# Performance work log

Hardware: AMD Instinct MI355X
Metric: run time of the kernel (lower is better)

## Reference

```python
import jax, jax.numpy as jnp
import numpy as np

LENGTHS = [1024, 768, 896, 512, 1024, 640, 1024, 768, 512, 896, 1024, 704]  # sum = 9792
EMBED, HEADS = 1024, 16
HDIM = EMBED // HEADS  # 64
ROPE_BASE = 10000.0


def _rotate_half(x):
    half = x.shape[-1] // 2
    return jnp.concatenate([-x[..., half:], x[..., :half]], axis=-1)


def setup_inputs() -> dict:
    key = jax.random.key(0)
    ks = jax.random.split(key, 8)
    T = sum(LENGTHS)
    hidden = jax.random.normal(ks[0], (T, EMBED), jnp.float32)
    # RoPE cos/sin: positions restart at 0 within each packed segment
    pos = np.concatenate([np.arange(l) for l in LENGTHS]).astype(np.float32)  # [T]
    inv_freq = 1.0 / (ROPE_BASE ** (np.arange(0, HDIM, 2, dtype=np.float32) / HDIM))
    freqs = np.outer(pos, inv_freq)                       # [T, HDIM//2]
    emb = np.concatenate([freqs, freqs], axis=-1)         # [T, HDIM]
    cos = jnp.asarray(np.cos(emb), jnp.float32)
    sin = jnp.asarray(np.sin(emb), jnp.float32)
    s = 0.02
    q_w = jax.random.normal(ks[1], (EMBED, EMBED), jnp.float32) * s
    k_w = jax.random.normal(ks[2], (EMBED, EMBED), jnp.float32) * s
    v_w = jax.random.normal(ks[3], (EMBED, EMBED), jnp.float32) * s
    out_w = jax.random.normal(ks[4], (EMBED, EMBED), jnp.float32) * s
    q_b = jax.random.normal(ks[5], (EMBED,), jnp.float32) * s
    v_b = jax.random.normal(ks[6], (EMBED,), jnp.float32) * s
    out_b = jax.random.normal(ks[7], (EMBED,), jnp.float32) * s
    return {
        "hidden_states": hidden, "cos": cos, "sin": sin,
        "q_w": q_w, "q_b": q_b, "k_w": k_w, "v_w": v_w, "v_b": v_b,
        "out_w": out_w, "out_b": out_b,
        "seq_len": jnp.array(LENGTHS, jnp.int32),
        "max_seqlen": 1024,
    }


def reference(hidden_states, cos, sin, q_w, q_b, k_w, v_w, v_b, out_w, out_b,
              seq_len, max_seqlen):
    T, D = hidden_states.shape
    H, Dh = HEADS, D // HEADS
    B = seq_len.shape[0]
    L = max_seqlen  # static python int

    # Projections (torch Linear: y = x @ W.T + b; k_proj has no bias)
    q = (hidden_states @ q_w.T + q_b).reshape(T, H, Dh)
    k = (hidden_states @ k_w.T).reshape(T, H, Dh)
    v = (hidden_states @ v_w.T + v_b).reshape(T, H, Dh)

    # Inline RoPE (cos/sin broadcast over heads)
    c = cos[:, None, :]
    s = sin[:, None, :]
    q = q * c + _rotate_half(q) * s
    k = k * c + _rotate_half(k) * s

    # Gather packed tokens into padded [B, L, H, Dh] (honors ragged structure:
    # no [T, T] dense score matrix, only per-segment [L, L] blocks)
    cu = jnp.concatenate([jnp.zeros((1,), seq_len.dtype), jnp.cumsum(seq_len)])[:-1]  # [B] starts
    ar = jnp.arange(L)
    idx = cu[:, None] + ar[None, :]                 # [B, L] token ids
    valid = ar[None, :] < seq_len[:, None]          # [B, L]
    idxc = jnp.minimum(idx, T - 1)
    qp = q[idxc]                                    # [B, L, H, Dh]
    kp = k[idxc]
    vp = v[idxc]

    scale = 1.0 / jnp.sqrt(jnp.float32(Dh))
    scores = jnp.einsum('blhd,bmhd->bhlm', qp, kp) * scale  # [B, H, L, L]
    causal = ar[:, None] >= ar[None, :]             # [L, L]
    mask = valid[:, None, None, :] & causal[None, None, :, :]
    scores = jnp.where(mask, scores, jnp.float32(-1e30))
    probs = jax.nn.softmax(scores, axis=-1)
    attn = jnp.einsum('bhlm,bmhd->blhd', probs, vp).reshape(B, L, D)

    # Scatter valid tokens back to packed layout [T, D]
    attn = attn * valid[..., None].astype(attn.dtype)
    flat = jnp.zeros((T, D), attn.dtype).at[idxc.reshape(-1)].add(attn.reshape(-1, D))
    return flat @ out_w.T + out_b
```

## Files before the change

### kernel.cpp

```cpp
#include <hip/hip_runtime.h>

typedef __bf16 bf16;
typedef __bf16 bf16x8 __attribute__((ext_vector_type(8)));
typedef __bf16 bf16x4 __attribute__((ext_vector_type(4)));
typedef float  f32x4  __attribute__((ext_vector_type(4)));

#define T_TOTAL 9792
#define EMBED   1024
#define NHEAD   16
#define HDIM    64

__constant__ int c_seq_start[12] = {0,1024,1792,2688,3200,4224,4864,5888,6656,7168,8064,9088};
__constant__ int c_tiles_cum[13] = {0,16,28,42,50,66,76,92,104,112,126,142,153};

typedef __attribute__((address_space(1))) unsigned int gu32;
typedef __attribute__((address_space(3))) unsigned int lu32;

__device__ __forceinline__ void load_lds16(const void* g, void* l) {
    __builtin_amdgcn_global_load_lds((gu32*)g, (lu32*)l, 16, 0, 0);
}

__device__ __forceinline__ f32x4 mfma16(bf16x8 a, bf16x8 b, f32x4 c) {
    return __builtin_amdgcn_mfma_f32_16x16x32_bf16(a, b, c, 0, 0, 0);
}

struct CvtArgs {
    const void* src[10];
    bf16*       dst[10];
    int         n[10];
    int         cum[10];
};

__global__ void to_bf16_fused(CvtArgs a, const unsigned short* __restrict__ disc)
{
    const bool f32 = (disc[0] == 0);
    const int blk = blockIdx.x;
    int seg = 0;
    #pragma unroll
    for (int i = 1; i < 10; ++i) if (blk >= a.cum[i]) seg = i;
    int i0 = (blk - a.cum[seg]) * 2048 + threadIdx.x * 8;
    if (i0 >= a.n[seg]) return;
    bf16x8 o;
    if (f32) {
        const float4* s = (const float4*)((const float*)a.src[seg] + i0);
        float4 x = s[0], y = s[1];
        o[0]=(bf16)x.x; o[1]=(bf16)x.y; o[2]=(bf16)x.z; o[3]=(bf16)x.w;
        o[4]=(bf16)y.x; o[5]=(bf16)y.y; o[6]=(bf16)y.z; o[7]=(bf16)y.w;
    } else {
        o = *(const bf16x8*)((const bf16*)a.src[seg] + i0);
    }
    *(bf16x8*)(a.dst[seg] + i0) = o;
}

__device__ __forceinline__
void gemm_core(const bf16* __restrict__ A, const bf16* __restrict__ W,
               int M, int m0, int n0, f32x4 (&acc)[4][4],
               bf16* lA, bf16* lB)
{
    const int tid  = threadIdx.x;
    const int wave = tid >> 6, lane = tid & 63;
    const int lrow = lane >> 3;
    const int gsw  = (lane & 7) ^ lrow;
    const int ln   = lane & 15, lq = lane >> 4;
    const int e7   = ln & 7;
    const int wm = (wave & 1) * 64,  wn = (wave >> 1) * 64;

    for (int k0 = 0; k0 < 1024; k0 += 64) {
        __syncthreads();
        for (int j = 0; j < 4; ++j) {
            int r = j * 32 + wave * 8;
            int gr = m0 + r + lrow; if (gr > M - 1) gr = M - 1;
            load_lds16(A + (size_t)gr * EMBED + k0 + gsw * 8, &lA[r * 64]);
            load_lds16(W + (size_t)(n0 + r + lrow) * EMBED + k0 + gsw * 8, &lB[r * 64]);
        }
        __syncthreads();
        #pragma unroll
        for (int kb = 0; kb < 2; ++kb) {
            bf16x8 af[4], bfr[4];
            #pragma unroll
            for (int i = 0; i < 4; ++i)
                af[i]  = *(const bf16x8*)&lA[(wm + i * 16 + ln) * 64 + (((kb * 4 + lq) ^ e7) * 8)];
            #pragma unroll
            for (int i = 0; i < 4; ++i)
                bfr[i] = *(const bf16x8*)&lB[(wn + i * 16 + ln) * 64 + (((kb * 4 + lq) ^ e7) * 8)];
            #pragma unroll
            for (int mi = 0; mi < 4; ++mi)
                #pragma unroll
                for (int ni = 0; ni < 4; ++ni)
                    acc[mi][ni] = mfma16(af[mi], bfr[ni], acc[mi][ni]);
        }
    }
}

__device__ __forceinline__ void map_block(int L, int NY, int& x, int& y)
{
    const int per = 8 * NY;
    const int full = 9 * per;
    if (L < full) { int sc = L / per, rem = L % per; x = sc * 8 + (rem & 7); y = rem >> 3; }
    else          { int rem = L - full; x = 72 + rem % 5; y = rem / 5; }
}

__global__ __launch_bounds__(256, 2)
void gemm_qkv(const bf16* __restrict__ A,
              const bf16* __restrict__ Wq, const bf16* __restrict__ Wk,
              const bf16* __restrict__ Wv, const bf16* __restrict__ qb,
              const bf16* __restrict__ vb,
              const bf16* __restrict__ cosb, const bf16* __restrict__ sinb,
              bf16* __restrict__ Cq, bf16* __restrict__ Ck,
              bf16* __restrict__ Vt, int M)
{
    __shared__ __align__(16) bf16 lA[128 * 64];
    __shared__ __align__(16) bf16 lB[128 * 64];

    int x, yy;
    map_block(blockIdx.x, 24, x, yy);
    const int which = yy >> 3;
    const int m0 = x * 128, n0 = (yy & 7) * 128;

    const bf16* W = (which == 0) ? Wq : (which == 1) ? Wk : Wv;
    f32x4 acc[4][4] = {};
    gemm_core(A, W, M, m0, n0, acc, lA, lB);

    const int tid  = threadIdx.x;
    const int wave = tid >> 6, lane = tid & 63;
    const int ln   = lane & 15, lq = lane >> 4;
    const int wm = (wave & 1) * 64,  wn = (wave >> 1) * 64;

    if (which < 2) {
        bf16* C = (which == 0) ? Cq : Ck;
        const bf16* bias = (which == 0) ? qb : nullptr;
        #pragma unroll
        for (int mi = 0; mi < 4; ++mi) {
            int trow = m0 + wm + mi * 16 + lq * 4;
            if (trow >= M) continue;
            #pragma unroll
            for (int ni = 0; ni < 2; ++ni) {
                int d    = ni * 16 + ln;
                int col0 = n0 + wn + d;
                int col1 = col0 + 32;
                float b0 = bias ? (float)bias[col0] : 0.0f;
                float b1 = bias ? (float)bias[col1] : 0.0f;
                #pragma unroll
                for (int r = 0; r < 4; ++r) {
                    int t = trow + r;
                    float c = (float)cosb[t * HDIM + d];
                    float s = (float)sinb[t * HDIM + d];
                    float x0 = acc[mi][ni][r] + b0;
                    float x1 = acc[mi][ni + 2][r] + b1;
                    C[(size_t)t * EMBED + col0] = (bf16)(x0 * c - x1 * s);
                    C[(size_t)t * EMBED + col1] = (bf16)(x1 * c + x0 * s);
                }
            }
        }
    } else {
        const int hd0 = n0 + wn;
        #pragma unroll
        for (int mi = 0; mi < 4; ++mi) {
            int trow = m0 + wm + mi * 16 + lq * 4;
            if (trow >= M) continue;
            #pragma unroll
            for (int ni = 0; ni < 4; ++ni) {
                int d = ni * 16 + ln;
                float bv = (float)vb[hd0 + d];
                bf16x4 o;
                #pragma unroll
                for (int r = 0; r < 4; ++r) o[r] = (bf16)(acc[mi][ni][r] + bv);
                *(bf16x4*)&Vt[(size_t)(hd0 + d) * T_TOTAL + trow] = o;
            }
        }
    }
}

__global__ __launch_bounds__(256, 2)
void gemm_out(const bf16* __restrict__ A, const bf16* __restrict__ W,
              const bf16* __restrict__ bias, void* __restrict__ out, int M,
              const unsigned short* __restrict__ disc)
{
    __shared__ __align__(16) bf16 lA[128 * 64];
    __shared__ __align__(16) bf16 lB[128 * 64];

    int x, yy;
    map_block(blockIdx.x, 8, x, yy);
    const int m0 = x * 128, n0 = yy * 128;

    f32x4 acc[4][4] = {};
    gemm_core(A, W, M, m0, n0, acc, lA, lB);

    const bool f32 = (disc[0] == 0);
    const int tid  = threadIdx.x;
    const int wave = tid >> 6, lane = tid & 63;
    const int ln   = lane & 15, lq = lane >> 4;
    const int wm = (wave & 1) * 64,  wn = (wave >> 1) * 64;

    #pragma unroll
    for (int mi = 0; mi < 4; ++mi) {
        int trow = m0 + wm + mi * 16 + lq * 4;
        if (trow >= M) continue;
        #pragma unroll
        for (int ni = 0; ni < 4; ++ni) {
            int col = n0 + wn + ni * 16 + ln;
            float bv = (float)bias[col];
            #pragma unroll
            for (int r = 0; r < 4; ++r) {
                float v = acc[mi][ni][r] + bv;
                size_t idx = (size_t)(trow + r) * EMBED + col;
                if (f32) ((float*)out)[idx] = v;
                else     ((bf16*)out)[idx]  = (bf16)v;
            }
        }
    }
}

__global__ __launch_bounds__(256, 3)
void attn_kernel(const bf16* __restrict__ Q, const bf16* __restrict__ K,
                 const bf16* __restrict__ Vt, bf16* __restrict__ O)
{
    __shared__ __align__(16) bf16 sK[2][64 * 64];
    __shared__ __align__(16) bf16 sV[2][64 * 64];
    __shared__ __align__(16) bf16 sQP[4 * 16 * 72];

    const int tid  = threadIdx.x;
    const int wave = tid >> 6, lane = tid & 63;
    const int lrow = lane >> 3;
    const int gsw  = (lane & 7) ^ lrow;
    const int ln   = lane & 15, lq = lane >> 4;
    const int e7   = ln & 7;
    const int h = blockIdx.y;

    int b = 0;
    #pragma unroll
    for (int i = 1; i < 13; ++i) if ((int)blockIdx.x >= c_tiles_cum[i]) b = i;
    const int qt = blockIdx.x - c_tiles_cum[b];
    const int t0 = c_seq_start[b] + qt * 64;
    const int kvb0 = c_seq_start[b];

    for (int p = 0; p < 2; ++p) {
        int r = p * 32 + wave * 8;
        load_lds16(Q  + (size_t)(t0 + r + lrow) * EMBED + h * HDIM + gsw * 8, &sQP[r * 64]);
        load_lds16(K  + (size_t)(kvb0 + r + lrow) * EMBED + h * HDIM + gsw * 8, &sK[0][r * 64]);
        load_lds16(Vt + (size_t)(h * HDIM + r + lrow) * T_TOTAL + kvb0 + gsw * 8, &sV[0][r * 64]);
    }

    bf16x8 qf[2];
    f32x4 oacc[4] = {};
    float m_i = -1e30f, l_i = 0.0f;
    const float sc = 0.125f * 1.44269504088896f;
    const int q_loc = wave * 16 + ln;
    bf16* sP = &sQP[wave * 16 * 72];

    for (int j = 0; j <= qt; ++j) {
        __syncthreads();
        const int cur = j & 1;
        if (j == 0) {
            qf[0] = *(const bf16x8*)&sQP[q_loc * 64 + ((0 + lq) ^ e7) * 8];
            qf[1] = *(const bf16x8*)&sQP[q_loc * 64 + ((4 + lq) ^ e7) * 8];
            __syncthreads();
        }
        if (j < qt) {
            const int kvb = kvb0 + (j + 1) * 64;
            const int nxt = cur ^ 1;
            for (int p = 0; p < 2; ++p) {
                int r = p * 32 + wave * 8;
                load_lds16(K  + (size_t)(kvb + r + lrow) * EMBED + h * HDIM + gsw * 8, &sK[nxt][r * 64]);
                load_lds16(Vt + (size_t)(h * HDIM + r + lrow) * T_TOTAL + kvb + gsw * 8, &sV[nxt][r * 64]);
            }
        }

        f32x4 s[4] = {};
        #pragma unroll
        for (int kk = 0; kk < 2; ++kk)
            #pragma unroll
            for (int ni = 0; ni < 4; ++ni) {
                bf16x8 kf = *(const bf16x8*)&sK[cur][(ni * 16 + ln) * 64 + (((kk * 4 + lq) ^ e7) * 8)];
                s[ni] = mfma16(kf, qf[kk], s[ni]);
            }

        float pb[4][4];
        if (j == qt) {
            #pragma unroll
            for (int ni = 0; ni < 4; ++ni)
                #pragma unroll
                for (int r = 0; r < 4; ++r) {
                    int kv = ni * 16 + lq * 4 + r;
                    pb[ni][r] = (kv <= q_loc) ? s[ni][r] * sc : -1e30f;
                }
        } else {
            #pragma unroll
            for (int ni = 0; ni < 4; ++ni)
                #pragma unroll
                for (int r = 0; r < 4; ++r)
                    pb[ni][r] = s[ni][r] * sc;
        }

        float mx = pb[0][0];
        #pragma unroll
        for (int ni = 0; ni < 4; ++ni)
            #pragma unroll
            for (int r = 0; r < 4; ++r) mx = fmaxf(mx, pb[ni][r]);
        mx = fmaxf(mx, __shfl_xor(mx, 16));
        mx = fmaxf(mx, __shfl_xor(mx, 32));
        float mnew  = fmaxf(m_i, mx);
        float alpha = exp2f(m_i - mnew);
        m_i = mnew;

        float rs = 0.0f;
        #pragma unroll
        for (int ni = 0; ni < 4; ++ni)
            #pragma unroll
            for (int r = 0; r < 4; ++r) {
                float pe = exp2f(pb[ni][r] - mnew);
                pb[ni][r] = pe;
                rs += pe;
            }
        rs += __shfl_xor(rs, 16);
        rs += __shfl_xor(rs, 32);
        l_i = l_i * alpha + rs;
        #pragma unroll
        for (int d = 0; d < 4; ++d)
            #pragma unroll
            for (int r = 0; r < 4; ++r) oacc[d][r] *= alpha;

        #pragma unroll
        for (int ni = 0; ni < 4; ++ni) {
            bf16x4 w4;
            #pragma unroll
            for (int r = 0; r < 4; ++r) w4[r] = (bf16)pb[ni][r];
            *(bf16x4*)&sP[ln * 72 + ni * 16 + lq * 4] = w4;
        }
        asm volatile("s_waitcnt lgkmcnt(0)" ::: "memory");

        #pragma unroll
        for (int kk = 0; kk < 2; ++kk) {
            bf16x8 pf = *(const bf16x8*)&sP[ln * 72 + kk * 32 + lq * 8];
            #pragma unroll
            for (int d = 0; d < 4; ++d) {
                bf16x8 vf = *(const bf16x8*)&sV[cur][(d * 16 + ln) * 64 + (((kk * 4 + lq) ^ e7) * 8)];
                oacc[d] = mfma16(vf, pf, oacc[d]);
            }
        }
    }

    const float inv = 1.0f / l_i;
    const size_t row = (size_t)(t0 + q_loc) * EMBED + h * HDIM;
    #pragma unroll
    for (int d = 0; d < 4; ++d) {
        bf16x4 o4;
        #pragma unroll
        for (int r = 0; r < 4; ++r) o4[r] = (bf16)(oacc[d][r] * inv);
        *(bf16x4*)&O[row + d * 16 + lq * 4] = o4;
    }
}

extern "C" void kernel_launch(void* const* d_in, const int* in_sizes, int n_in,
                              void* d_out, int out_size, void* d_ws, size_t ws_size,
                              hipStream_t stream)
{
    const unsigned short* disc = (const unsigned short*)d_in[1];

    const size_t SZ  = (size_t)T_TOTAL * EMBED;
    const size_t CS  = (size_t)T_TOTAL * HDIM;
    const size_t WSZ = (size_t)EMBED * EMBED;

    bf16* p = (bf16*)d_ws;
    bf16* ch   = p; p += SZ;
    bf16* ccos = p; p += CS;
    bf16* csin = p; p += CS;
    bf16* cqw  = p; p += WSZ;
    bf16* ckw  = p; p += WSZ;
    bf16* cvw  = p; p += WSZ;
    bf16* cow  = p; p += WSZ;
    bf16* cqb  = p; p += EMBED;
    bf16* cvb  = p; p += EMBED;
    bf16* cob  = p; p += EMBED;
    bf16* wq   = p; p += SZ;
    bf16* wk   = p; p += SZ;
    bf16* wvt  = p; p += SZ;

    CvtArgs ca;
    const void* srcs[10] = {d_in[0], d_in[1], d_in[2], d_in[3], d_in[5],
                            d_in[6], d_in[8], d_in[4], d_in[7], d_in[9]};
    bf16* dsts[10] = {ch, ccos, csin, cqw, ckw, cvw, cow, cqb, cvb, cob};
    int   ns[10]   = {(int)SZ, (int)CS, (int)CS, (int)WSZ, (int)WSZ,
                      (int)WSZ, (int)WSZ, EMBED, EMBED, EMBED};
    int cum = 0;
    for (int i = 0; i < 10; ++i) {
        ca.src[i] = srcs[i]; ca.dst[i] = dsts[i]; ca.n[i] = ns[i];
        ca.cum[i] = cum;
        cum += (ns[i] + 2047) / 2048;
    }
    to_bf16_fused<<<cum, 256, 0, stream>>>(ca, disc);

    gemm_qkv<<<77 * 24, 256, 0, stream>>>(ch, cqw, ckw, cvw, cqb, cvb,
                                          ccos, csin, wq, wk, wvt, T_TOTAL);
    attn_kernel<<<dim3(153, 16), 256, 0, stream>>>(wq, wk, wvt, wq);
    gemm_out<<<77 * 8, 256, 0, stream>>>(wq, cow, cob, d_out, T_TOTAL, disc);
}
```

Baseline: 283.5 us.

## Process 128 query rows per attention block, remap GEMM tiles, add nontemporal IO

The attention kernel now assigns 128 query rows per block, with each wave handling two 16-row sub-tiles. This lets the K/V tiles loaded into shared memory be reused across twice as many queries, and the grid shrinks to half the blocks. Causal skipping and masking move to a per-sub-tile granularity. The GEMM block-to-tile mapping is simplified with a separate Q/K/V stride, and the conversion and output kernels use nontemporal loads and stores. The trade-offs are larger per-block work, higher register use, and possibly worse load balance across CUs.

```diff
diff --git a/kernel.cpp b/kernel.cpp
--- a/kernel.cpp
+++ b/kernel.cpp
@@ -10,8 +10,9 @@
 #define NHEAD   16
 #define HDIM    64
 
-__constant__ int c_seq_start[12] = {0,1024,1792,2688,3200,4224,4864,5888,6656,7168,8064,9088};
-__constant__ int c_tiles_cum[13] = {0,16,28,42,50,66,76,92,104,112,126,142,153};
+__constant__ int c_seq_start[12]  = {0,1024,1792,2688,3200,4224,4864,5888,6656,7168,8064,9088};
+__constant__ int c_tiles2_cum[13] = {0,8,14,21,25,33,38,46,52,56,63,71,77};
+__constant__ int c_len64[12]      = {16,12,14,8,16,10,16,12,8,14,16,11};
 
 typedef __attribute__((address_space(1))) unsigned int gu32;
 typedef __attribute__((address_space(3))) unsigned int lu32;
@@ -42,10 +43,11 @@
     if (i0 >= a.n[seg]) return;
     bf16x8 o;
     if (f32) {
-        const float4* s = (const float4*)((const float*)a.src[seg] + i0);
-        float4 x = s[0], y = s[1];
-        o[0]=(bf16)x.x; o[1]=(bf16)x.y; o[2]=(bf16)x.z; o[3]=(bf16)x.w;
-        o[4]=(bf16)y.x; o[5]=(bf16)y.y; o[6]=(bf16)y.z; o[7]=(bf16)y.w;
+        const f32x4* s = (const f32x4*)((const float*)a.src[seg] + i0);
+        f32x4 x = __builtin_nontemporal_load(s);
+        f32x4 y = __builtin_nontemporal_load(s + 1);
+        o[0]=(bf16)x[0]; o[1]=(bf16)x[1]; o[2]=(bf16)x[2]; o[3]=(bf16)x[3];
+        o[4]=(bf16)y[0]; o[5]=(bf16)y[1]; o[6]=(bf16)y[2]; o[7]=(bf16)y[3];
     } else {
         o = *(const bf16x8*)((const bf16*)a.src[seg] + i0);
     }
@@ -92,12 +94,10 @@
     }
 }
 
-__device__ __forceinline__ void map_block(int L, int NY, int& x, int& y)
-{
-    const int per = 8 * NY;
-    const int full = 9 * per;
-    if (L < full) { int sc = L / per, rem = L % per; x = sc * 8 + (rem & 7); y = rem >> 3; }
-    else          { int rem = L - full; x = 72 + rem % 5; y = rem / 5; }
+__device__ __forceinline__ void map_sc(int r, int& x, int& y)
+{
+    if (r < 576) { int sc = r >> 6, q = r & 63; x = sc * 8 + (q & 7); y = q >> 3; }
+    else         { int r2 = r - 576; x = 72 + (r2 % 5); y = r2 / 5; }
 }
 
 __global__ __launch_bounds__(256, 2)
@@ -112,10 +112,10 @@
     __shared__ __align__(16) bf16 lA[128 * 64];
     __shared__ __align__(16) bf16 lB[128 * 64];
 
+    const int which = blockIdx.x / 616;
     int x, yy;
-    map_block(blockIdx.x, 24, x, yy);
-    const int which = yy >> 3;
-    const int m0 = x * 128, n0 = (yy & 7) * 128;
+    map_sc(blockIdx.x - which * 616, x, yy);
+    const int m0 = x * 128, n0 = yy * 128;
 
     const bf16* W = (which == 0) ? Wq : (which == 1) ? Wk : Wv;
     f32x4 acc[4][4] = {};
@@ -180,7 +180,7 @@
     __shared__ __align__(16) bf16 lB[128 * 64];
 
     int x, yy;
-    map_block(blockIdx.x, 8, x, yy);
+    map_sc(blockIdx.x, x, yy);
     const int m0 = x * 128, n0 = yy * 128;
 
     f32x4 acc[4][4] = {};
@@ -204,8 +204,8 @@
             for (int r = 0; r < 4; ++r) {
                 float v = acc[mi][ni][r] + bv;
                 size_t idx = (size_t)(trow + r) * EMBED + col;
-                if (f32) ((float*)out)[idx] = v;
-                else     ((bf16*)out)[idx]  = (bf16)v;
+                if (f32) __builtin_nontemporal_store(v, (float*)out + idx);
+                else     __builtin_nontemporal_store((bf16)v, (bf16*)out + idx);
             }
         }
     }
@@ -217,7 +217,7 @@
 {
     __shared__ __align__(16) bf16 sK[2][64 * 64];
     __shared__ __align__(16) bf16 sV[2][64 * 64];
-    __shared__ __align__(16) bf16 sQP[4 * 16 * 72];
+    __shared__ __align__(16) bf16 sQP[4 * 32 * 72];
 
     const int tid  = threadIdx.x;
     const int wave = tid >> 6, lane = tid & 63;
@@ -229,35 +229,43 @@
 
     int b = 0;
     #pragma unroll
-    for (int i = 1; i < 13; ++i) if ((int)blockIdx.x >= c_tiles_cum[i]) b = i;
-    const int qt = blockIdx.x - c_tiles_cum[b];
-    const int t0 = c_seq_start[b] + qt * 64;
-    const int kvb0 = c_seq_start[b];
-
+    for (int i = 1; i < 13; ++i) if ((int)blockIdx.x >= c_tiles2_cum[i]) b = i;
+    const int qt2 = blockIdx.x - c_tiles2_cum[b];
+    const int s0  = c_seq_start[b];
+    const int Q0r = qt2 * 128;
+    const int nb  = c_len64[b];
+    const int jmax = min(2 * qt2 + 1, nb - 1);
+
+    for (int p = 0; p < 4; ++p) {
+        int r = p * 32 + wave * 8;
+        int gr = s0 + Q0r + r + lrow; if (gr > T_TOTAL - 1) gr = T_TOTAL - 1;
+        load_lds16(Q + (size_t)gr * EMBED + h * HDIM + gsw * 8, &sQP[r * 64]);
+    }
     for (int p = 0; p < 2; ++p) {
         int r = p * 32 + wave * 8;
-        load_lds16(Q  + (size_t)(t0 + r + lrow) * EMBED + h * HDIM + gsw * 8, &sQP[r * 64]);
-        load_lds16(K  + (size_t)(kvb0 + r + lrow) * EMBED + h * HDIM + gsw * 8, &sK[0][r * 64]);
-        load_lds16(Vt + (size_t)(h * HDIM + r + lrow) * T_TOTAL + kvb0 + gsw * 8, &sV[0][r * 64]);
-    }
-
-    bf16x8 qf[2];
-    f32x4 oacc[4] = {};
-    float m_i = -1e30f, l_i = 0.0f;
+        load_lds16(K  + (size_t)(s0 + r + lrow) * EMBED + h * HDIM + gsw * 8, &sK[0][r * 64]);
+        load_lds16(Vt + (size_t)(h * HDIM + r + lrow) * T_TOTAL + s0 + gsw * 8, &sV[0][r * 64]);
+    }
+    __syncthreads();
+
+    bf16x8 qf[2][2];
+    #pragma unroll
+    for (int s = 0; s < 2; ++s)
+        #pragma unroll
+        for (int kk = 0; kk < 2; ++kk)
+            qf[s][kk] = *(const bf16x8*)&sQP[(wave * 32 + s * 16 + ln) * 64 + ((kk * 4 + lq) ^ e7) * 8];
+    __syncthreads();
+
+    f32x4 oacc[2][4] = {};
+    float m_i[2] = {-1e30f, -1e30f}, l_i[2] = {0.0f, 0.0f};
     const float sc = 0.125f * 1.44269504088896f;
-    const int q_loc = wave * 16 + ln;
-    bf16* sP = &sQP[wave * 16 * 72];
-
-    for (int j = 0; j <= qt; ++j) {
-        __syncthreads();
+    const int qmin0 = Q0r + wave * 32;
+    bf16* sPw = &sQP[wave * 32 * 72];
+
+    for (int j = 0; j <= jmax; ++j) {
         const int cur = j & 1;
-        if (j == 0) {
-            qf[0] = *(const bf16x8*)&sQP[q_loc * 64 + ((0 + lq) ^ e7) * 8];
-            qf[1] = *(const bf16x8*)&sQP[q_loc * 64 + ((4 + lq) ^ e7) * 8];
-            __syncthreads();
-        }
-        if (j < qt) {
-            const int kvb = kvb0 + (j + 1) * 64;
+        if (j < jmax) {
+            const int kvb = s0 + (j + 1) * 64;
             const int nxt = cur ^ 1;
             for (int p = 0; p < 2; ++p) {
                 int r = p * 32 + wave * 8;
@@ -266,88 +274,113 @@
             }
         }
 
-        f32x4 s[4] = {};
+        const int kv0 = j * 64;
+        const bool act0 = (kv0 <= qmin0 + 15);
+        const bool act1 = (kv0 <= qmin0 + 31);
+
+        bf16x8 kf[2][4];
         #pragma unroll
         for (int kk = 0; kk < 2; ++kk)
             #pragma unroll
+            for (int ni = 0; ni < 4; ++ni)
+                kf[kk][ni] = *(const bf16x8*)&sK[cur][(ni * 16 + ln) * 64 + ((kk * 4 + lq) ^ e7) * 8];
+
+        #pragma unroll
+        for (int s = 0; s < 2; ++s) {
+            if (!(s ? act1 : act0)) continue;
+            const int qmin = qmin0 + s * 16;
+
+            f32x4 sa[4] = {};
+            #pragma unroll
+            for (int kk = 0; kk < 2; ++kk)
+                #pragma unroll
+                for (int ni = 0; ni < 4; ++ni)
+                    sa[ni] = mfma16(kf[kk][ni], qf[s][kk], sa[ni]);
+
+            float pb[4][4];
+            if (kv0 + 63 > qmin) {
+                int qloc = qmin + ln;
+                #pragma unroll
+                for (int ni = 0; ni < 4; ++ni)
+                    #pragma unroll
+                    for (int r = 0; r < 4; ++r) {
+                        int kv = kv0 + ni * 16 + lq * 4 + r;
+                        pb[ni][r] = (kv <= qloc) ? sa[ni][r] * sc : -1e30f;
+                    }
+            } else {
+                #pragma unroll
+                for (int ni = 0; ni < 4; ++ni)
+                    #pragma unroll
+                    for (int r = 0; r < 4; ++r)
+                        pb[ni][r] = sa[ni][r] * sc;
+            }
+
+            float mx = pb[0][0];
+            #pragma unroll
+            for (int ni = 0; ni < 4; ++ni)
+                #pragma unroll
+                for (int r = 0; r < 4; ++r) mx = fmaxf(mx, pb[ni][r]);
+            mx = fmaxf(mx, __shfl_xor(mx, 16));
+            mx = fmaxf(mx, __shfl_xor(mx, 32));
+            float mnew  = fmaxf(m_i[s], mx);
+            float alpha = exp2f(m_i[s] - mnew);
+            m_i[s] = mnew;
+
+            float rs = 0.0f;
+            #pragma unroll
+            for (int ni = 0; ni < 4; ++ni)
+                #pragma unroll
+                for (int r = 0; r < 4; ++r) {
+                    float pe = exp2f(pb[ni][r] - mnew);
+                    pb[ni][r] = pe;
+                    rs += pe;
+                }
+            rs += __shfl_xor(rs, 16);
+            rs += __shfl_xor(rs, 32);
+            l_i[s] = l_i[s] * alpha + rs;
+            #pragma unroll
+            for (int d = 0; d < 4; ++d)
+                #pragma unroll
+                for (int r = 0; r < 4; ++r) oacc[s][d][r] *= alpha;
+
+            #pragma unroll
             for (int ni = 0; ni < 4; ++ni) {
-                bf16x8 kf = *(const bf16x8*)&sK[cur][(ni * 16 + ln) * 64 + (((kk * 4 + lq) ^ e7) * 8)];
-                s[ni] = mfma16(kf, qf[kk], s[ni]);
-            }
-
-        float pb[4][4];
-        if (j == qt) {
-            #pragma unroll
-            for (int ni = 0; ni < 4; ++ni)
-                #pragma unroll
-                for (int r = 0; r < 4; ++r) {
-                    int kv = ni * 16 + lq * 4 + r;
-                    pb[ni][r] = (kv <= q_loc) ? s[ni][r] * sc : -1e30f;
-                }
-        } else {
-            #pragma unroll
-            for (int ni = 0; ni < 4; ++ni)
-                #pragma unroll
-                for (int r = 0; r < 4; ++r)
-                    pb[ni][r] = s[ni][r] * sc;
-        }
-
-        float mx = pb[0][0];
-        #pragma unroll
-        for (int ni = 0; ni < 4; ++ni)
-            #pragma unroll
-            for (int r = 0; r < 4; ++r) mx = fmaxf(mx, pb[ni][r]);
-        mx = fmaxf(mx, __shfl_xor(mx, 16));
-        mx = fmaxf(mx, __shfl_xor(mx, 32));
-        float mnew  = fmaxf(m_i, mx);
-        float alpha = exp2f(m_i - mnew);
-        m_i = mnew;
-
-        float rs = 0.0f;
-        #pragma unroll
-        for (int ni = 0; ni < 4; ++ni)
-            #pragma unroll
-            for (int r = 0; r < 4; ++r) {
-                float pe = exp2f(pb[ni][r] - mnew);
-                pb[ni][r] = pe;
-                rs += pe;
-            }
-        rs += __shfl_xor(rs, 16);
-        rs += __shfl_xor(rs, 32);
-        l_i = l_i * alpha + rs;
-        #pragma unroll
-        for (int d = 0; d < 4; ++d)
-            #pragma unroll
-            for (int r = 0; r < 4; ++r) oacc[d][r] *= alpha;
-
-        #pragma unroll
-        for (int ni = 0; ni < 4; ++ni) {
-            bf16x4 w4;
-            #pragma unroll
-            for (int r = 0; r < 4; ++r) w4[r] = (bf16)pb[ni][r];
-            *(bf16x4*)&sP[ln * 72 + ni * 16 + lq * 4] = w4;
+                bf16x4 w4;
+                #pragma unroll
+                for (int r = 0; r < 4; ++r) w4[r] = (bf16)pb[ni][r];
+                *(bf16x4*)&sPw[(s * 16 + ln) * 72 + ni * 16 + lq * 4] = w4;
+            }
         }
         asm volatile("s_waitcnt lgkmcnt(0)" ::: "memory");
 
         #pragma unroll
         for (int kk = 0; kk < 2; ++kk) {
-            bf16x8 pf = *(const bf16x8*)&sP[ln * 72 + kk * 32 + lq * 8];
+            bf16x8 pf0, pf1;
+            if (act0) pf0 = *(const bf16x8*)&sPw[(0 * 16 + ln) * 72 + kk * 32 + lq * 8];
+            if (act1) pf1 = *(const bf16x8*)&sPw[(1 * 16 + ln) * 72 + kk * 32 + lq * 8];
             #pragma unroll
             for (int d = 0; d < 4; ++d) {
-                bf16x8 vf = *(const bf16x8*)&sV[cur][(d * 16 + ln) * 64 + (((kk * 4 + lq) ^ e7) * 8)];
-                oacc[d] = mfma16(vf, pf, oacc[d]);
-            }
-        }
-    }
-
-    const float inv = 1.0f / l_i;
-    const size_t row = (size_t)(t0 + q_loc) * EMBED + h * HDIM;
+                bf16x8 vf = *(const bf16x8*)&sV[cur][(d * 16 + ln) * 64 + ((kk * 4 + lq) ^ e7) * 8];
+                if (act0) oacc[0][d] = mfma16(vf, pf0, oacc[0][d]);
+                if (act1) oacc[1][d] = mfma16(vf, pf1, oacc[1][d]);
+            }
+        }
+        __syncthreads();
+    }
+
     #pragma unroll
-    for (int d = 0; d < 4; ++d) {
-        bf16x4 o4;
-        #pragma unroll
-        for (int r = 0; r < 4; ++r) o4[r] = (bf16)(oacc[d][r] * inv);
-        *(bf16x4*)&O[row + d * 16 + lq * 4] = o4;
+    for (int s = 0; s < 2; ++s) {
+        int qg = s0 + Q0r + wave * 32 + s * 16 + ln;
+        if (qg >= T_TOTAL) continue;
+        const float inv = 1.0f / l_i[s];
+        const size_t base = (size_t)qg * EMBED + h * HDIM;
+        #pragma unroll
+        for (int d = 0; d < 4; ++d) {
+            bf16x4 o4;
+            #pragma unroll
+            for (int r = 0; r < 4; ++r) o4[r] = (bf16)(oacc[s][d][r] * inv);
+            *(bf16x4*)&O[base + d * 16 + lq * 4] = o4;
+        }
     }
 }
 
@@ -390,8 +423,8 @@
     }
     to_bf16_fused<<<cum, 256, 0, stream>>>(ca, disc);
 
-    gemm_qkv<<<77 * 24, 256, 0, stream>>>(ch, cqw, ckw, cvw, cqb, cvb,
+    gemm_qkv<<<3 * 616, 256, 0, stream>>>(ch, cqw, ckw, cvw, cqb, cvb,
                                           ccos, csin, wq, wk, wvt, T_TOTAL);
-    attn_kernel<<<dim3(153, 16), 256, 0, stream>>>(wq, wk, wvt, wq);
-    gemm_out<<<77 * 8, 256, 0, stream>>>(wq, cow, cob, d_out, T_TOTAL, disc);
-}
+    attn_kernel<<<dim3(77, 16), 256, 0, stream>>>(wq, wk, wvt, wq);
+    gemm_out<<<616, 256, 0, stream>>>(wq, cow, cob, d_out, T_TOTAL, disc);
+}
```

Result: slower. 303.8 us (+7.2%).

## Schedule attention tiles longest-first and regroup QKV GEMM blocks by weight matrix

Applied to the files above, without the earlier changes.

The attention grid now reads a constant table that orders query tiles by descending causal work, so the longest tiles launch first and the tail is better balanced. The QKV GEMM grid is regrouped so each weight matrix (Q, K, V) gets a contiguous range of blocks, using a simpler supertile mapping. It also adds nontemporal loads in the fp32-to-bf16 conversion and nontemporal stores in the output GEMM, to cut cache pollution from streaming data. The work is unchanged; the risks are worse L2 reuse of the shared activations across Q/K/V and possible cache interactions from the nontemporal hints.

```diff
diff --git a/kernel.cpp b/kernel.cpp
--- a/kernel.cpp
+++ b/kernel.cpp
@@ -11,7 +11,25 @@
 #define HDIM    64
 
 __constant__ int c_seq_start[12] = {0,1024,1792,2688,3200,4224,4864,5888,6656,7168,8064,9088};
-__constant__ int c_tiles_cum[13] = {0,16,28,42,50,66,76,92,104,112,126,142,153};
+
+__constant__ unsigned char c_order[153] = {
+  240,244,246,250,
+  224,228,230,234,
+  208,210,212,214,217,218,
+  192,194,196,198,201,202,
+  176,177,178,180,182,183,185,186,
+  160,161,162,164,166,167,169,170,171,
+  144,145,146,148,149,150,151,153,154,155,
+  128,129,130,132,133,134,135,137,138,139,
+  112,113,114,115,116,117,118,119,120,121,122,123,
+  96,97,98,99,100,101,102,103,104,105,106,107,
+  80,81,82,83,84,85,86,87,88,89,90,91,
+  64,65,66,67,68,69,70,71,72,73,74,75,
+  48,49,50,51,52,53,54,55,56,57,58,59,
+  32,33,34,35,36,37,38,39,40,41,42,43,
+  16,17,18,19,20,21,22,23,24,25,26,27,
+  0,1,2,3,4,5,6,7,8,9,10,11
+};
 
 typedef __attribute__((address_space(1))) unsigned int gu32;
 typedef __attribute__((address_space(3))) unsigned int lu32;
@@ -42,10 +60,11 @@
     if (i0 >= a.n[seg]) return;
     bf16x8 o;
     if (f32) {
-        const float4* s = (const float4*)((const float*)a.src[seg] + i0);
-        float4 x = s[0], y = s[1];
-        o[0]=(bf16)x.x; o[1]=(bf16)x.y; o[2]=(bf16)x.z; o[3]=(bf16)x.w;
-        o[4]=(bf16)y.x; o[5]=(bf16)y.y; o[6]=(bf16)y.z; o[7]=(bf16)y.w;
+        const f32x4* s = (const f32x4*)((const float*)a.src[seg] + i0);
+        f32x4 x = __builtin_nontemporal_load(s);
+        f32x4 y = __builtin_nontemporal_load(s + 1);
+        o[0]=(bf16)x[0]; o[1]=(bf16)x[1]; o[2]=(bf16)x[2]; o[3]=(bf16)x[3];
+        o[4]=(bf16)y[0]; o[5]=(bf16)y[1]; o[6]=(bf16)y[2]; o[7]=(bf16)y[3];
     } else {
         o = *(const bf16x8*)((const bf16*)a.src[seg] + i0);
     }
@@ -92,12 +111,10 @@
     }
 }
 
-__device__ __forceinline__ void map_block(int L, int NY, int& x, int& y)
-{
-    const int per = 8 * NY;
-    const int full = 9 * per;
-    if (L < full) { int sc = L / per, rem = L % per; x = sc * 8 + (rem & 7); y = rem >> 3; }
-    else          { int rem = L - full; x = 72 + rem % 5; y = rem / 5; }
+__device__ __forceinline__ void map_sc(int r, int& x, int& y)
+{
+    if (r < 576) { int sc = r >> 6, q = r & 63; x = sc * 8 + (q & 7); y = q >> 3; }
+    else         { int r2 = r - 576; x = 72 + (r2 % 5); y = r2 / 5; }
 }
 
 __global__ __launch_bounds__(256, 2)
@@ -112,10 +129,10 @@
     __shared__ __align__(16) bf16 lA[128 * 64];
     __shared__ __align__(16) bf16 lB[128 * 64];
 
+    const int which = blockIdx.x / 616;
     int x, yy;
-    map_block(blockIdx.x, 24, x, yy);
-    const int which = yy >> 3;
-    const int m0 = x * 128, n0 = (yy & 7) * 128;
+    map_sc(blockIdx.x - which * 616, x, yy);
+    const int m0 = x * 128, n0 = yy * 128;
 
     const bf16* W = (which == 0) ? Wq : (which == 1) ? Wk : Wv;
     f32x4 acc[4][4] = {};
@@ -180,7 +197,7 @@
     __shared__ __align__(16) bf16 lB[128 * 64];
 
     int x, yy;
-    map_block(blockIdx.x, 8, x, yy);
+    map_sc(blockIdx.x, x, yy);
     const int m0 = x * 128, n0 = yy * 128;
 
     f32x4 acc[4][4] = {};
@@ -204,8 +221,8 @@
             for (int r = 0; r < 4; ++r) {
                 float v = acc[mi][ni][r] + bv;
                 size_t idx = (size_t)(trow + r) * EMBED + col;
-                if (f32) ((float*)out)[idx] = v;
-                else     ((bf16*)out)[idx]  = (bf16)v;
+                if (f32) __builtin_nontemporal_store(v, (float*)out + idx);
+                else     __builtin_nontemporal_store((bf16)v, (bf16*)out + idx);
             }
         }
     }
@@ -227,10 +244,9 @@
     const int e7   = ln & 7;
     const int h = blockIdx.y;
 
-    int b = 0;
-    #pragma unroll
-    for (int i = 1; i < 13; ++i) if ((int)blockIdx.x >= c_tiles_cum[i]) b = i;
-    const int qt = blockIdx.x - c_tiles_cum[b];
+    const int code = c_order[blockIdx.x];
+    const int b  = code & 15;
+    const int qt = code >> 4;
     const int t0 = c_seq_start[b] + qt * 64;
     const int kvb0 = c_seq_start[b];
 
@@ -271,7 +287,7 @@
         for (int kk = 0; kk < 2; ++kk)
             #pragma unroll
             for (int ni = 0; ni < 4; ++ni) {
-                bf16x8 kf = *(const bf16x8*)&sK[cur][(ni * 16 + ln) * 64 + (((kk * 4 + lq) ^ e7) * 8)];
+                bf16x8 kf = *(const bf16x8*)&sK[cur][(ni * 16 + ln) * 64 + ((kk * 4 + lq) ^ e7) * 8];
                 s[ni] = mfma16(kf, qf[kk], s[ni]);
             }
 
@@ -334,7 +350,7 @@
             bf16x8 pf = *(const bf16x8*)&sP[ln * 72 + kk * 32 + lq * 8];
             #pragma unroll
             for (int d = 0; d < 4; ++d) {
-                bf16x8 vf = *(const bf16x8*)&sV[cur][(d * 16 + ln) * 64 + (((kk * 4 + lq) ^ e7) * 8)];
+                bf16x8 vf = *(const bf16x8*)&sV[cur][(d * 16 + ln) * 64 + ((kk * 4 + lq) ^ e7) * 8];
                 oacc[d] = mfma16(vf, pf, oacc[d]);
             }
         }
@@ -390,8 +406,8 @@
     }
     to_bf16_fused<<<cum, 256, 0, stream>>>(ca, disc);
 
-    gemm_qkv<<<77 * 24, 256, 0, stream>>>(ch, cqw, ckw, cvw, cqb, cvb,
+    gemm_qkv<<<3 * 616, 256, 0, stream>>>(ch, cqw, ckw, cvw, cqb, cvb,
                                           ccos, csin, wq, wk, wvt, T_TOTAL);
     attn_kernel<<<dim3(153, 16), 256, 0, stream>>>(wq, wk, wvt, wq);
-    gemm_out<<<77 * 8, 256, 0, stream>>>(wq, cow, cob, d_out, T_TOTAL, disc);
-}
+    gemm_out<<<616, 256, 0, stream>>>(wq, cow, cob, d_out, T_TOTAL, disc);
+}
```

Result: slower. 294.6 us (+3.9%).
